# Kernel tuning notes

Hardware: AMD Instinct MI355X
Metric: run time of the kernel (lower is better)

Reference implementation:

```python
import jax, jax.numpy as jnp
import numpy as np

N = 50000      # nodes
R = 4          # relations
E = 1600000    # edges per relation
IN = 256       # in_feats
H = 256        # h_feats
C = 16         # num_classes


def setup_inputs() -> dict:
    key = jax.random.key(0)
    ks = jax.random.split(key, 8)
    X = jax.random.normal(ks[0], (N, IN), jnp.float32)
    edge_index = jax.random.randint(ks[1], (R, 2, E), 0, N, dtype=jnp.int32)
    W1 = jax.random.normal(ks[2], (R, IN, H), jnp.float32) * (1.0 / np.sqrt(IN))
    W2 = jax.random.normal(ks[3], (R, H, H), jnp.float32) * (1.0 / np.sqrt(H))
    att_q = jax.random.normal(ks[4], (H,), jnp.float32) * (1.0 / np.sqrt(H))
    tau = jnp.asarray(2.0, jnp.float32)
    W_out = jax.random.normal(ks[5], (H, C), jnp.float32) * (1.0 / np.sqrt(H))
    b_out = jnp.zeros((C,), jnp.float32)
    return {"X": X, "edge_index": edge_index, "W1": W1, "W2": W2,
            "att_q": att_q, "tau": tau, "W_out": W_out, "b_out": b_out}


def _sym_norm_spmm(edge, feat):
    """out = D^{-1/2} A D^{-1/2} @ feat for one relation, edge: [2,E]."""
    row, col = edge[0], edge[1]
    ones = jnp.ones(edge.shape[1], feat.dtype)
    deg_r = jax.ops.segment_sum(ones, row, num_segments=N)
    deg_c = jax.ops.segment_sum(ones, col, num_segments=N)
    dinv_r = jax.lax.rsqrt(jnp.maximum(deg_r, 1.0))
    dinv_c = jax.lax.rsqrt(jnp.maximum(deg_c, 1.0))
    w = dinv_r[row] * dinv_c[col]                      # [E]
    msg = w[:, None] * feat[col]                       # gather + scale
    return jax.ops.segment_sum(msg, row, num_segments=N)  # [N, F]


def _rel_layer(edge_index, feat, W):
    # vmapped over relations: ReLU(A_r feat W_r) -> [R, N, H]
    def one(edge, Wr):
        return jax.nn.relu(_sym_norm_spmm(edge, feat) @ Wr)
    return jax.vmap(one)(edge_index, W)


def reference(X, edge_index, W1, W2, att_q, tau, W_out, b_out):
    # Layer 1: mean over relations (eval mode: no dropout)
    H1 = _rel_layer(edge_index, X, W1)        # [R, N, H]
    h1 = H1.mean(axis=0)                      # [N, H]
    # Layer 2 with relation attention
    H2 = _rel_layer(edge_index, h1, W2)       # [R, N, H]
    scores = jnp.einsum('rnh,h->nr', H2, att_q)
    tau_c = jnp.clip(tau, 0.5, 5.0)
    alpha = jax.nn.softmax(scores / tau_c, axis=1)   # [N, R]
    h2_att = jnp.einsum('nr,rnh->nh', alpha, H2)
    h2 = H2.mean(axis=0) + h2_att             # residual fusion
    logits = h2 @ W_out + b_out               # [N, C]
    return logits, alpha
```

## Files before the change

### kernel.cpp

```cpp
#include <hip/hip_runtime.h>
#include <hip/hip_bf16.h>
#include <stdint.h>

#define NODES 50000
#define RELS  4
#define EDGES 1600000
#define FEAT  256
#define NCLS  16
#define MPAD  50048
#define RPS   50016
#define NCHUNK 64
#define CHUNKE 25000
#define NB     782

typedef __attribute__((ext_vector_type(8))) short short8;
typedef __attribute__((ext_vector_type(8))) unsigned short u16x8;
typedef __attribute__((ext_vector_type(4))) float f32x4;

static __device__ __forceinline__ float bf2f(unsigned short u) {
    return __uint_as_float(((unsigned int)u) << 16);
}
static __device__ __forceinline__ unsigned short f2bf(float f) {
    unsigned int x = __float_as_uint(f);
    unsigned int r = x + 0x7fffu + ((x >> 16) & 1u);
    return (unsigned short)(r >> 16);
}


__global__ __launch_bounds__(256)
void k_bhist2(const int* __restrict__ edges, unsigned* __restrict__ partR,
              unsigned* __restrict__ partC) {
    int chunk = blockIdx.x, rel = blockIdx.y, t = threadIdx.x;
    const int* rows = edges + (size_t)rel * 2 * EDGES + (size_t)chunk * CHUNKE;
    const int* cols = rows + EDGES;
    __shared__ unsigned hR[NB];
    __shared__ unsigned hC[NB];
    for (int i = t; i < NB; i += 256) { hR[i] = 0; hC[i] = 0; }
    __syncthreads();
    for (int e = t; e < CHUNKE; e += 256) {
        atomicAdd(&hR[((unsigned)rows[e]) >> 6], 1u);
        atomicAdd(&hC[((unsigned)cols[e]) >> 6], 1u);
    }
    __syncthreads();
    unsigned* pR = partR + ((size_t)rel * NCHUNK + chunk) * NB;
    unsigned* pC = partC + ((size_t)rel * NCHUNK + chunk) * NB;
    for (int i = t; i < NB; i += 256) { pR[i] = hR[i]; pC[i] = hC[i]; }
}

__global__ __launch_bounds__(256)
void k_bscan(const unsigned* __restrict__ partR, unsigned* __restrict__ offR,
             unsigned* __restrict__ bbR, const unsigned* __restrict__ partC,
             unsigned* __restrict__ offC, unsigned* __restrict__ bbC) {
    int rel = blockIdx.x & 3, t = threadIdx.x;
    const unsigned* part = (blockIdx.x < 4) ? partR : partC;
    unsigned* off   = (blockIdx.x < 4) ? offR : offC;
    unsigned* bbase = (blockIdx.x < 4) ? bbR  : bbC;
    const int BPT = 4;
    int b0 = t * BPT;
    unsigned s = 0;
#pragma unroll
    for (int j = 0; j < BPT; ++j) {
        int b = b0 + j;
        unsigned x = 0;
        if (b < NB)
            for (int c = 0; c < NCHUNK; ++c)
                x += part[((size_t)rel * NCHUNK + c) * NB + b];
        s += x;
    }
    __shared__ unsigned sh[256];
    sh[t] = s;
    __syncthreads();
    for (int o = 1; o < 256; o <<= 1) {
        unsigned u = (t >= o) ? sh[t - o] : 0;
        __syncthreads();
        sh[t] += u;
        __syncthreads();
    }
    unsigned base = sh[t] - s;
#pragma unroll
    for (int j = 0; j < BPT; ++j) {
        int b = b0 + j;
        if (b < NB) {
            bbase[rel * (NB + 1) + b] = base;
            unsigned acc = base;
            for (int c = 0; c < NCHUNK; ++c) {
                size_t o2 = ((size_t)rel * NCHUNK + c) * NB + b;
                off[o2] = acc;
                acc += part[o2];
            }
            base = acc;
        }
    }
    if (t == 255) bbase[rel * (NB + 1) + NB] = sh[255];
}

__global__ __launch_bounds__(256)
void k_scat2(const int* __restrict__ edges, const unsigned* __restrict__ offR,
             const unsigned* __restrict__ offC, unsigned* __restrict__ ebuf,
             unsigned char* __restrict__ cbuf) {
    int chunk = blockIdx.x, rel = blockIdx.y, t = threadIdx.x;
    const int* rows = edges + (size_t)rel * 2 * EDGES + (size_t)chunk * CHUNKE;
    const int* cols = rows + EDGES;
    __shared__ unsigned curR[NB];
    __shared__ unsigned curC[NB];
    const unsigned* pR = offR + ((size_t)rel * NCHUNK + chunk) * NB;
    const unsigned* pC = offC + ((size_t)rel * NCHUNK + chunk) * NB;
    for (int i = t; i < NB; i += 256) { curR[i] = pR[i]; curC[i] = pC[i]; }
    __syncthreads();
    unsigned*      eb = ebuf + (size_t)rel * EDGES;
    unsigned char* cb = cbuf + (size_t)rel * EDGES;
    for (int e = t; e < CHUNKE; e += 256) {
        int r = rows[e], c = cols[e];
        unsigned pr = atomicAdd(&curR[((unsigned)r) >> 6], 1u);
        eb[pr] = (((unsigned)(r & 63)) << 16) | (unsigned)c;
        unsigned pc = atomicAdd(&curC[((unsigned)c) >> 6], 1u);
        cb[pc] = (unsigned char)(c & 63);
    }
}

__global__ __launch_bounds__(256)
void k_finish(const unsigned* __restrict__ ebuf, const unsigned char* __restrict__ cbuf,
              const unsigned* __restrict__ bbR, const unsigned* __restrict__ bbC,
              int* __restrict__ csr_col, int* __restrict__ row_ptr,
              float* __restrict__ dinv_row, float* __restrict__ dinv_col) {
    int b = blockIdx.x, rel = blockIdx.y, t = threadIdx.x;
    unsigned sR = bbR[rel * (NB + 1) + b], eR = bbR[rel * (NB + 1) + b + 1];
    unsigned sC = bbC[rel * (NB + 1) + b], eC = bbC[rel * (NB + 1) + b + 1];
    __shared__ unsigned rcnt[64];
    __shared__ unsigned ccnt[64];
    __shared__ int cur[64];
    if (t < 64) { rcnt[t] = 0; ccnt[t] = 0; }
    __syncthreads();
    const unsigned*      eb = ebuf + (size_t)rel * EDGES;
    const unsigned char* cb = cbuf + (size_t)rel * EDGES;
    for (unsigned i = sR + t; i < eR; i += 256) atomicAdd(&rcnt[eb[i] >> 16], 1u);
    for (unsigned i = sC + t; i < eC; i += 256) atomicAdd(&ccnt[cb[i]], 1u);
    __syncthreads();
    int base = b * 64;
    if (t < 64) {
        unsigned c = rcnt[t];
        unsigned v = c;
#pragma unroll
        for (int off = 1; off < 64; off <<= 1) {
            unsigned n = __shfl_up(v, off, 64);
            if (t >= off) v += n;
        }
        unsigned excl = v - c;
        cur[t] = (int)(sR + excl);
        if (base + t < NODES) {
            row_ptr[rel * RPS + base + t] = (int)(sR + excl);
            int d = (int)c; if (d < 1) d = 1;
            dinv_row[(size_t)rel * NODES + base + t] = rsqrtf((float)d);
        }
        if (b == 0 && t == 0) row_ptr[rel * RPS + NODES] = EDGES;
    } else if (t >= 64 && t < 128) {
        int tt = t - 64;
        if (base + tt < NODES) {
            int d = (int)ccnt[tt]; if (d < 1) d = 1;
            dinv_col[(size_t)rel * NODES + base + tt] = rsqrtf((float)d);
        }
    }
    __syncthreads();
    int* cc = csr_col + (size_t)rel * EDGES;
    for (unsigned i = sR + t; i < eR; i += 256) {
        unsigned v = eb[i];
        int pos = atomicAdd(&cur[v >> 16], 1);
        cc[pos] = (int)(v & 0xFFFFu);
    }
}


#define WELEMS (2 * RELS * FEAT * FEAT)
#define XGROUPS (NODES * FEAT / 8)

__global__ __launch_bounds__(256)
void k_conv(const float* __restrict__ W1, const float* __restrict__ W2,
            unsigned short* __restrict__ W1t, unsigned short* __restrict__ W2t,
            const float* __restrict__ X, unsigned short* __restrict__ Xbf) {
    int gid = blockIdx.x * 256 + threadIdx.x;
    if (gid < WELEMS) {
        const int half = RELS * FEAT * FEAT;
        const float* W = (gid < half) ? W1 : W2;
        unsigned short* Wt = (gid < half) ? W1t : W2t;
        int id = (gid < half) ? gid : gid - half;
        int r = id >> 16;
        int rem = id & 65535;
        int n = rem >> 8;
        int k = rem & 255;
        Wt[id] = f2bf(W[(size_t)r * FEAT * FEAT + (size_t)k * FEAT + n]);
        return;
    }
    int i = gid - WELEMS;
    if (i >= XGROUPS) return;
    const float* s = X + (size_t)i * 8;
    float4 a = *(const float4*)s;
    float4 b = *(const float4*)(s + 4);
    u16x8 v;
    v[0] = f2bf(a.x); v[1] = f2bf(a.y); v[2] = f2bf(a.z); v[3] = f2bf(a.w);
    v[4] = f2bf(b.x); v[5] = f2bf(b.y); v[6] = f2bf(b.z); v[7] = f2bf(b.w);
    *(u16x8*)(Xbf + (size_t)i * 8) = v;
}


__global__ __launch_bounds__(256)
void k_spmm(const unsigned short* __restrict__ feat, const int* __restrict__ row_ptr,
            const int* __restrict__ csr_col, const float* __restrict__ dinv_row,
            const float* __restrict__ dinv_col, unsigned short* __restrict__ aggbase,
            int slice_off) {
    int rel = blockIdx.y;
    unsigned short* aggbf = aggbase + (size_t)(rel + slice_off) * (size_t)MPAD * FEAT;
    int wave = (blockIdx.x * blockDim.x + threadIdx.x) >> 6;
    int lane = threadIdx.x & 63;
    if (wave >= NODES) return;
    int row = wave;
    int half = lane >> 5;
    int l32  = lane & 31;
    int start = row_ptr[rel * RPS + row];
    int end   = row_ptr[rel * RPS + row + 1];
    const int* cols = csr_col + (size_t)rel * EDGES;
    const float* dc = dinv_col + rel * NODES;
    const unsigned short* fb = feat + l32 * 8;
    float acc[8] = {0.f, 0.f, 0.f, 0.f, 0.f, 0.f, 0.f, 0.f};
    int j = start + half;
    for (; j + 2 < end; j += 4) {
        int c0 = cols[j];
        int c1 = cols[j + 2];
        float w0 = dc[c0];
        float w1 = dc[c1];
        u16x8 u0 = *(const u16x8*)(fb + (size_t)c0 * FEAT);
        u16x8 u1 = *(const u16x8*)(fb + (size_t)c1 * FEAT);
#pragma unroll
        for (int i = 0; i < 8; ++i) acc[i] += w0 * bf2f(u0[i]);
#pragma unroll
        for (int i = 0; i < 8; ++i) acc[i] += w1 * bf2f(u1[i]);
    }
    if (j < end) {
        int c0 = cols[j];
        float w0 = dc[c0];
        u16x8 u0 = *(const u16x8*)(fb + (size_t)c0 * FEAT);
#pragma unroll
        for (int i = 0; i < 8; ++i) acc[i] += w0 * bf2f(u0[i]);
    }
#pragma unroll
    for (int i = 0; i < 8; ++i) acc[i] += __shfl_down(acc[i], 32, 64);
    if (half == 0) {
        float dr = dinv_row[rel * NODES + row];
        u16x8 o;
#pragma unroll
        for (int i = 0; i < 8; ++i) o[i] = f2bf(acc[i] * dr);
        *(u16x8*)(aggbf + (size_t)row * FEAT + l32 * 8) = o;
    }
}


__global__ __launch_bounds__(256)
void k_gemm1(const unsigned short* __restrict__ Abase, const unsigned short* __restrict__ Wt,
             unsigned short* __restrict__ h1bf) {
    __shared__ __align__(16) unsigned short As[128 * 64];
    __shared__ __align__(16) unsigned short Bs[128 * 64];
    int tid = threadIdx.x;
    int wave = tid >> 6, lane = tid & 63;
    int quad = lane >> 4, l16 = lane & 15;
    int wm = (wave & 1) * 64, wn = (wave >> 1) * 64;
    int row0 = blockIdx.x * 128, n0 = blockIdx.y * 128;

    f32x4 hacc[4][4];
#pragma unroll
    for (int mi = 0; mi < 4; ++mi)
#pragma unroll
        for (int ni = 0; ni < 4; ++ni)
            hacc[mi][ni] = (f32x4){0.f, 0.f, 0.f, 0.f};

    for (int r = 0; r < RELS; ++r) {
        const unsigned short* A  = Abase + (size_t)r * MPAD * FEAT;
        const unsigned short* Bt = Wt + (size_t)r * FEAT * FEAT;
        f32x4 acc[4][4];
#pragma unroll
        for (int mi = 0; mi < 4; ++mi)
#pragma unroll
            for (int ni = 0; ni < 4; ++ni)
                acc[mi][ni] = (f32x4){0.f, 0.f, 0.f, 0.f};

        for (int k0 = 0; k0 < FEAT; k0 += 64) {
#pragma unroll
            for (int issue = 0; issue < 4; ++issue) {
                int flat = issue * 256 + tid;
                int row = flat >> 3;
                int gr = flat & 7;
                int sg = gr ^ (row & 7);
                *(uint4*)&As[flat * 8] = *(const uint4*)(A + (size_t)(row0 + row) * FEAT + k0 + sg * 8);
                *(uint4*)&Bs[flat * 8] = *(const uint4*)(Bt + (size_t)(n0 + row) * FEAT + k0 + sg * 8);
            }
            __syncthreads();
#pragma unroll
            for (int ks = 0; ks < 2; ++ks) {
                int g = ks * 4 + quad;
                short8 af[4], bfr[4];
#pragma unroll
                for (int mi = 0; mi < 4; ++mi) {
                    int m = wm + mi * 16 + l16;
                    af[mi] = *(const short8*)&As[m * 64 + ((g ^ (m & 7)) << 3)];
                }
#pragma unroll
                for (int ni = 0; ni < 4; ++ni) {
                    int n = wn + ni * 16 + l16;
                    bfr[ni] = *(const short8*)&Bs[n * 64 + ((g ^ (n & 7)) << 3)];
                }
#pragma unroll
                for (int mi = 0; mi < 4; ++mi)
#pragma unroll
                    for (int ni = 0; ni < 4; ++ni)
                        acc[mi][ni] = __builtin_amdgcn_mfma_f32_16x16x32_bf16(af[mi], bfr[ni], acc[mi][ni], 0, 0, 0);
            }
            __syncthreads();
        }
#pragma unroll
        for (int mi = 0; mi < 4; ++mi)
#pragma unroll
            for (int ni = 0; ni < 4; ++ni)
#pragma unroll
                for (int i = 0; i < 4; ++i) {
                    float v = acc[mi][ni][i];
                    hacc[mi][ni][i] += 0.25f * (v > 0.f ? v : 0.f);
                }
    }

#pragma unroll
    for (int mi = 0; mi < 4; ++mi)
#pragma unroll
        for (int ni = 0; ni < 4; ++ni) {
            int col = n0 + wn + ni * 16 + l16;
#pragma unroll
            for (int i = 0; i < 4; ++i) {
                int row = row0 + wm + mi * 16 + quad * 4 + i;
                if (row < NODES) h1bf[(size_t)row * FEAT + col] = f2bf(hacc[mi][ni][i]);
            }
        }
}

__global__ __launch_bounds__(256)
void k_gemm2z(const unsigned short* __restrict__ aggbase, const unsigned short* __restrict__ Wtb,
              unsigned short* __restrict__ o0, unsigned short* __restrict__ o1,
              unsigned short* __restrict__ o2, unsigned short* __restrict__ o3) {
    __shared__ __align__(16) unsigned short As[128 * 64];
    __shared__ __align__(16) unsigned short Bs[128 * 64];
    int rz = blockIdx.z;
    const unsigned short* A  = aggbase + (size_t)(rz + 1) * MPAD * FEAT;
    const unsigned short* Bt = Wtb + (size_t)rz * FEAT * FEAT;
    unsigned short* H2 = (rz == 0) ? o0 : (rz == 1) ? o1 : (rz == 2) ? o2 : o3;

    int tid = threadIdx.x;
    int wave = tid >> 6, lane = tid & 63;
    int quad = lane >> 4, l16 = lane & 15;
    int wm = (wave & 1) * 64, wn = (wave >> 1) * 64;
    int row0 = blockIdx.x * 128, n0 = blockIdx.y * 128;

    f32x4 acc[4][4];
#pragma unroll
    for (int mi = 0; mi < 4; ++mi)
#pragma unroll
        for (int ni = 0; ni < 4; ++ni)
            acc[mi][ni] = (f32x4){0.f, 0.f, 0.f, 0.f};

    for (int k0 = 0; k0 < FEAT; k0 += 64) {
#pragma unroll
        for (int issue = 0; issue < 4; ++issue) {
            int flat = issue * 256 + tid;
            int row = flat >> 3;
            int gr = flat & 7;
            int sg = gr ^ (row & 7);
            *(uint4*)&As[flat * 8] = *(const uint4*)(A + (size_t)(row0 + row) * FEAT + k0 + sg * 8);
            *(uint4*)&Bs[flat * 8] = *(const uint4*)(Bt + (size_t)(n0 + row) * FEAT + k0 + sg * 8);
        }
        __syncthreads();
#pragma unroll
        for (int ks = 0; ks < 2; ++ks) {
            int g = ks * 4 + quad;
            short8 af[4], bfr[4];
#pragma unroll
            for (int mi = 0; mi < 4; ++mi) {
                int m = wm + mi * 16 + l16;
                af[mi] = *(const short8*)&As[m * 64 + ((g ^ (m & 7)) << 3)];
            }
#pragma unroll
            for (int ni = 0; ni < 4; ++ni) {
                int n = wn + ni * 16 + l16;
                bfr[ni] = *(const short8*)&Bs[n * 64 + ((g ^ (n & 7)) << 3)];
            }
#pragma unroll
            for (int mi = 0; mi < 4; ++mi)
#pragma unroll
                for (int ni = 0; ni < 4; ++ni)
                    acc[mi][ni] = __builtin_amdgcn_mfma_f32_16x16x32_bf16(af[mi], bfr[ni], acc[mi][ni], 0, 0, 0);
        }
        __syncthreads();
    }

#pragma unroll
    for (int mi = 0; mi < 4; ++mi)
#pragma unroll
        for (int ni = 0; ni < 4; ++ni) {
            int col = n0 + wn + ni * 16 + l16;
#pragma unroll
            for (int i = 0; i < 4; ++i) {
                int row = row0 + wm + mi * 16 + quad * 4 + i;
                if (row < NODES) {
                    float v = acc[mi][ni][i];
                    H2[(size_t)row * FEAT + col] = f2bf(v > 0.f ? v : 0.f);
                }
            }
        }
}


__global__ __launch_bounds__(256)
void k_attn_out(const unsigned short* __restrict__ p0, const unsigned short* __restrict__ p1,
                const unsigned short* __restrict__ p2, const unsigned short* __restrict__ p3,
                const float* __restrict__ att_q, const float* __restrict__ tau_p,
                const float* __restrict__ W_out, const float* __restrict__ b_out,
                float* __restrict__ alpha_out, float* __restrict__ logits) {
    __shared__ float red[4][64 * 17];
    int tid = threadIdx.x;
    int wid = tid >> 6;
    int lane = tid & 63;
    int gwave = blockIdx.x * 4 + wid;
    int nwaves = gridDim.x * 4;

    const unsigned short* hp[RELS] = {p0, p1, p2, p3};
    float4 q = *(const float4*)(att_q + lane * 4);
    float tau = fminf(fmaxf(tau_p[0], 0.5f), 5.0f);
    float itau = 1.0f / tau;
    f32x4 Wr[4][4];
#pragma unroll
    for (int j = 0; j < 4; ++j)
#pragma unroll
        for (int c4 = 0; c4 < 4; ++c4) {
            float4 w = *(const float4*)(W_out + (size_t)(lane * 4 + j) * NCLS + c4 * 4);
            Wr[j][c4] = (f32x4){w.x, w.y, w.z, w.w};
        }
    float bc = b_out[lane & 15];
    float* myred = &red[wid][0];
    int cls = lane & 15;
    int rb = (lane >> 4) * 16;

    int n = gwave;
    if (n >= NODES) return;
    ushort4 u[RELS];
#pragma unroll
    for (int r = 0; r < RELS; ++r)
        u[r] = *(const ushort4*)(hp[r] + (size_t)n * FEAT + lane * 4);

    while (n < NODES) {
        int nn = n + nwaves;
        int nc = (nn < NODES) ? nn : n;
        ushort4 un[RELS];
#pragma unroll
        for (int r = 0; r < RELS; ++r)
            un[r] = *(const ushort4*)(hp[r] + (size_t)nc * FEAT + lane * 4);

        float h[RELS][4];
#pragma unroll
        for (int r = 0; r < RELS; ++r) {
            h[r][0] = bf2f(u[r].x); h[r][1] = bf2f(u[r].y);
            h[r][2] = bf2f(u[r].z); h[r][3] = bf2f(u[r].w);
        }
        float s[RELS];
#pragma unroll
        for (int r = 0; r < RELS; ++r)
            s[r] = h[r][0] * q.x + h[r][1] * q.y + h[r][2] * q.z + h[r][3] * q.w;
#pragma unroll
        for (int off = 1; off < 64; off <<= 1) {
#pragma unroll
            for (int r = 0; r < RELS; ++r) s[r] += __shfl_xor(s[r], off, 64);
        }
        float m = fmaxf(fmaxf(s[0], s[1]), fmaxf(s[2], s[3]));
        float e[RELS];
        float esum = 0.f;
#pragma unroll
        for (int r = 0; r < RELS; ++r) { e[r] = expf((s[r] - m) * itau); esum += e[r]; }
        float inv = 1.0f / esum;
        float a[RELS];
#pragma unroll
        for (int r = 0; r < RELS; ++r) a[r] = e[r] * inv;
        if (lane == 0)
            *(float4*)(alpha_out + (size_t)n * 4) = make_float4(a[0], a[1], a[2], a[3]);

        float w0 = 0.25f + a[0], w1 = 0.25f + a[1], w2 = 0.25f + a[2], w3 = 0.25f + a[3];
        float h2[4];
#pragma unroll
        for (int j = 0; j < 4; ++j)
            h2[j] = w0 * h[0][j] + w1 * h[1][j] + w2 * h[2][j] + w3 * h[3][j];

        f32x4 acc[4];
#pragma unroll
        for (int c4 = 0; c4 < 4; ++c4)
            acc[c4] = h2[0] * Wr[0][c4] + h2[1] * Wr[1][c4]
                    + h2[2] * Wr[2][c4] + h2[3] * Wr[3][c4];

#pragma unroll
        for (int c4 = 0; c4 < 4; ++c4)
#pragma unroll
            for (int i = 0; i < 4; ++i)
                myred[lane * 17 + c4 * 4 + i] = acc[c4][i];
        asm volatile("s_waitcnt lgkmcnt(0)" ::: "memory");
        float t = 0.f;
#pragma unroll
        for (int k = 0; k < 16; ++k) t += myred[(rb + k) * 17 + cls];
        t += __shfl_xor(t, 16, 64);
        t += __shfl_xor(t, 32, 64);
        if (lane < 16) logits[(size_t)n * NCLS + lane] = t + bc;
        asm volatile("" ::: "memory");

#pragma unroll
        for (int r = 0; r < RELS; ++r) u[r] = un[r];
        n = nn;
    }
}


static inline int cdiv(int a, int b) { return (a + b - 1) / b; }

extern "C" void kernel_launch(void* const* d_in, const int* in_sizes, int n_in,
                              void* d_out, int out_size, void* d_ws, size_t ws_size,
                              hipStream_t stream) {
    const float* X     = (const float*)d_in[0];
    const int*   edges = (const int*)d_in[1];
    const float* W1    = (const float*)d_in[2];
    const float* W2    = (const float*)d_in[3];
    const float* att_q = (const float*)d_in[4];
    const float* tau   = (const float*)d_in[5];
    const float* W_out = (const float*)d_in[6];
    const float* b_out = (const float*)d_in[7];

    float* logits = (float*)d_out;
    float* alpha  = logits + (size_t)NODES * NCLS;

    char* p = (char*)d_ws;
    auto carve = [&](size_t bytes) -> char* {
        char* q = p;
        p += (bytes + 255) & ~(size_t)255;
        return q;
    };
    float* dinv_row = (float*)carve((size_t)RELS * NODES * 4);
    float* dinv_col = (float*)carve((size_t)RELS * NODES * 4);
    int*   row_ptr  = (int*)carve((size_t)RELS * RPS * 4 + 256);
    int*   csr_col  = (int*)carve((size_t)RELS * EDGES * 4);
    unsigned short* Xbf  = (unsigned short*)carve((size_t)NODES * FEAT * 2);
    unsigned short* h1bf = (unsigned short*)carve((size_t)NODES * FEAT * 2);
    unsigned short* W1t  = (unsigned short*)carve((size_t)RELS * FEAT * FEAT * 2);
    unsigned short* W2t  = (unsigned short*)carve((size_t)RELS * FEAT * FEAT * 2);
    const size_t AGGSE = (size_t)MPAD * FEAT;
    char* BIG = carve(5 * AGGSE * 2);
    unsigned*      ebuf = (unsigned*)BIG;
    unsigned char* cbuf = (unsigned char*)(BIG + (size_t)RELS * EDGES * 4);
    char*     q = BIG + (size_t)RELS * EDGES * 5;
    q = (char*)(((uintptr_t)q + 255) & ~(uintptr_t)255);
    unsigned* partR = (unsigned*)q;               q += (size_t)RELS * NCHUNK * NB * 4;
    unsigned* offR  = (unsigned*)q;               q += (size_t)RELS * NCHUNK * NB * 4;
    unsigned* partC = (unsigned*)q;               q += (size_t)RELS * NCHUNK * NB * 4;
    unsigned* offC  = (unsigned*)q;               q += (size_t)RELS * NCHUNK * NB * 4;
    unsigned* bbR   = (unsigned*)q;               q += (size_t)RELS * (NB + 1) * 4;
    unsigned* bbC   = (unsigned*)q;
    unsigned short* aggbf = (unsigned short*)BIG;
    unsigned short* H2_0 = aggbf;
    unsigned short* H2_1 = Xbf;
    unsigned short* H2_2 = h1bf;
    unsigned short* H2_3 = (unsigned short*)csr_col;

    {
        dim3 hg(NCHUNK, RELS);
        dim3 bg(NB, RELS);
        k_bhist2<<<hg, 256, 0, stream>>>(edges, partR, partC);
        k_bscan<<<8, 256, 0, stream>>>(partR, offR, bbR, partC, offC, bbC);
        k_scat2<<<hg, 256, 0, stream>>>(edges, offR, offC, ebuf, cbuf);
        k_finish<<<bg, 256, 0, stream>>>(ebuf, cbuf, bbR, bbC, csr_col, row_ptr,
                                         dinv_row, dinv_col);
    }

    k_conv<<<cdiv(WELEMS + XGROUPS, 256), 256, 0, stream>>>(W1, W2, W1t, W2t, X, Xbf);

    dim3 gemm_grid(MPAD / 128, FEAT / 128);
    dim3 gemm2_grid(MPAD / 128, FEAT / 128, RELS);
    dim3 spmm_grid(cdiv(NODES * 64, 256), RELS);

    k_spmm<<<spmm_grid, 256, 0, stream>>>(Xbf, row_ptr, csr_col, dinv_row, dinv_col,
                                          aggbf, 0);
    k_gemm1<<<gemm_grid, 256, 0, stream>>>(aggbf, W1t, h1bf);

    k_spmm<<<spmm_grid, 256, 0, stream>>>(h1bf, row_ptr, csr_col, dinv_row, dinv_col,
                                          aggbf, 1);
    k_gemm2z<<<gemm2_grid, 256, 0, stream>>>(aggbf, W2t, H2_0, H2_1, H2_2, H2_3);

    k_attn_out<<<1024, 256, 0, stream>>>(H2_0, H2_1, H2_2, H2_3, att_q, tau,
                                         W_out, b_out, alpha, logits);
}
```

Measured before the change: 1.379 ms.

## Fuse conversion into histogram kernel, double chunk count, use direct global-to-LDS loads

The weight/feature bf16 conversion kernel is merged into the edge histogram launch as extra blocks, removing one launch and letting conversion overlap with histogramming. The edge chunk count is doubled (half-size chunks) to raise parallelism in the histogram and scatter passes. The GEMM tile loads switch from register-staged copies to the global_load_lds builtin to cut VGPR traffic. Risks: more partial histograms for the scan to handle, and the LDS direct-load path depends on correct layout and synchronization.

```diff
diff --git a/kernel.cpp b/kernel.cpp
--- a/kernel.cpp
+++ b/kernel.cpp
@@ -9,9 +9,13 @@
 #define NCLS  16
 #define MPAD  50048
 #define RPS   50016
-#define NCHUNK 64
-#define CHUNKE 25000
+#define NCHUNK 128
+#define CHUNKE 12500
 #define NB     782
+
+#define WELEMS (2 * RELS * FEAT * FEAT)
+#define XGROUPS (NODES * FEAT / 8)
+#define CONVB  2075
 
 typedef __attribute__((ext_vector_type(8))) short short8;
 typedef __attribute__((ext_vector_type(8))) unsigned short u16x8;
@@ -26,15 +30,50 @@
     return (unsigned short)(r >> 16);
 }
 
+#define GLOAD_LDS16(gsrc, ldst)                                                          \
+    __builtin_amdgcn_global_load_lds(                                                    \
+        (const __attribute__((address_space(1))) unsigned int*)(gsrc),                   \
+        (__attribute__((address_space(3))) unsigned int*)(ldst), 16, 0, 0)
+
 
 __global__ __launch_bounds__(256)
 void k_bhist2(const int* __restrict__ edges, unsigned* __restrict__ partR,
-              unsigned* __restrict__ partC) {
-    int chunk = blockIdx.x, rel = blockIdx.y, t = threadIdx.x;
+              unsigned* __restrict__ partC,
+              const float* __restrict__ W1, const float* __restrict__ W2,
+              unsigned short* __restrict__ W1t, unsigned short* __restrict__ W2t,
+              const float* __restrict__ X, unsigned short* __restrict__ Xbf) {
+    __shared__ unsigned hR[NB];
+    __shared__ unsigned hC[NB];
+    int t = threadIdx.x;
+    if (blockIdx.x >= NCHUNK) {
+        int cid = (blockIdx.x - NCHUNK) * RELS + blockIdx.y;
+        int gid = cid * 256 + t;
+        if (gid < WELEMS) {
+            const int half = RELS * FEAT * FEAT;
+            const float* W = (gid < half) ? W1 : W2;
+            unsigned short* Wt = (gid < half) ? W1t : W2t;
+            int id = (gid < half) ? gid : gid - half;
+            int r = id >> 16;
+            int rem = id & 65535;
+            int n = rem >> 8;
+            int k = rem & 255;
+            Wt[id] = f2bf(W[(size_t)r * FEAT * FEAT + (size_t)k * FEAT + n]);
+            return;
+        }
+        int i = gid - WELEMS;
+        if (i >= XGROUPS) return;
+        const float* s = X + (size_t)i * 8;
+        float4 a = *(const float4*)s;
+        float4 b = *(const float4*)(s + 4);
+        u16x8 v;
+        v[0] = f2bf(a.x); v[1] = f2bf(a.y); v[2] = f2bf(a.z); v[3] = f2bf(a.w);
+        v[4] = f2bf(b.x); v[5] = f2bf(b.y); v[6] = f2bf(b.z); v[7] = f2bf(b.w);
+        *(u16x8*)(Xbf + (size_t)i * 8) = v;
+        return;
+    }
+    int chunk = blockIdx.x, rel = blockIdx.y;
     const int* rows = edges + (size_t)rel * 2 * EDGES + (size_t)chunk * CHUNKE;
     const int* cols = rows + EDGES;
-    __shared__ unsigned hR[NB];
-    __shared__ unsigned hC[NB];
     for (int i = t; i < NB; i += 256) { hR[i] = 0; hC[i] = 0; }
     __syncthreads();
     for (int e = t; e < CHUNKE; e += 256) {
@@ -167,38 +206,6 @@
         int pos = atomicAdd(&cur[v >> 16], 1);
         cc[pos] = (int)(v & 0xFFFFu);
     }
-}
-
-
-#define WELEMS (2 * RELS * FEAT * FEAT)
-#define XGROUPS (NODES * FEAT / 8)
-
-__global__ __launch_bounds__(256)
-void k_conv(const float* __restrict__ W1, const float* __restrict__ W2,
-            unsigned short* __restrict__ W1t, unsigned short* __restrict__ W2t,
-            const float* __restrict__ X, unsigned short* __restrict__ Xbf) {
-    int gid = blockIdx.x * 256 + threadIdx.x;
-    if (gid < WELEMS) {
-        const int half = RELS * FEAT * FEAT;
-        const float* W = (gid < half) ? W1 : W2;
-        unsigned short* Wt = (gid < half) ? W1t : W2t;
-        int id = (gid < half) ? gid : gid - half;
-        int r = id >> 16;
-        int rem = id & 65535;
-        int n = rem >> 8;
-        int k = rem & 255;
-        Wt[id] = f2bf(W[(size_t)r * FEAT * FEAT + (size_t)k * FEAT + n]);
-        return;
-    }
-    int i = gid - WELEMS;
-    if (i >= XGROUPS) return;
-    const float* s = X + (size_t)i * 8;
-    float4 a = *(const float4*)s;
-    float4 b = *(const float4*)(s + 4);
-    u16x8 v;
-    v[0] = f2bf(a.x); v[1] = f2bf(a.y); v[2] = f2bf(a.z); v[3] = f2bf(a.w);
-    v[4] = f2bf(b.x); v[5] = f2bf(b.y); v[6] = f2bf(b.z); v[7] = f2bf(b.w);
-    *(u16x8*)(Xbf + (size_t)i * 8) = v;
 }
 
 
@@ -288,8 +295,8 @@
                 int row = flat >> 3;
                 int gr = flat & 7;
                 int sg = gr ^ (row & 7);
-                *(uint4*)&As[flat * 8] = *(const uint4*)(A + (size_t)(row0 + row) * FEAT + k0 + sg * 8);
-                *(uint4*)&Bs[flat * 8] = *(const uint4*)(Bt + (size_t)(n0 + row) * FEAT + k0 + sg * 8);
+                GLOAD_LDS16(A + (size_t)(row0 + row) * FEAT + k0 + sg * 8, &As[flat * 8]);
+                GLOAD_LDS16(Bt + (size_t)(n0 + row) * FEAT + k0 + sg * 8, &Bs[flat * 8]);
             }
             __syncthreads();
 #pragma unroll
@@ -369,8 +376,8 @@
             int row = flat >> 3;
             int gr = flat & 7;
             int sg = gr ^ (row & 7);
-            *(uint4*)&As[flat * 8] = *(const uint4*)(A + (size_t)(row0 + row) * FEAT + k0 + sg * 8);
-            *(uint4*)&Bs[flat * 8] = *(const uint4*)(Bt + (size_t)(n0 + row) * FEAT + k0 + sg * 8);
+            GLOAD_LDS16(A + (size_t)(row0 + row) * FEAT + k0 + sg * 8, &As[flat * 8]);
+            GLOAD_LDS16(Bt + (size_t)(n0 + row) * FEAT + k0 + sg * 8, &Bs[flat * 8]);
         }
         __syncthreads();
 #pragma unroll
@@ -568,16 +575,15 @@
     unsigned short* H2_3 = (unsigned short*)csr_col;
 
     {
-        dim3 hg(NCHUNK, RELS);
+        dim3 hg(NCHUNK + CONVB, RELS);
+        dim3 sg(NCHUNK, RELS);
         dim3 bg(NB, RELS);
-        k_bhist2<<<hg, 256, 0, stream>>>(edges, partR, partC);
+        k_bhist2<<<hg, 256, 0, stream>>>(edges, partR, partC, W1, W2, W1t, W2t, X, Xbf);
         k_bscan<<<8, 256, 0, stream>>>(partR, offR, bbR, partC, offC, bbC);
-        k_scat2<<<hg, 256, 0, stream>>>(edges, offR, offC, ebuf, cbuf);
+        k_scat2<<<sg, 256, 0, stream>>>(edges, offR, offC, ebuf, cbuf);
         k_finish<<<bg, 256, 0, stream>>>(ebuf, cbuf, bbR, bbC, csr_col, row_ptr,
                                          dinv_row, dinv_col);
     }
-
-    k_conv<<<cdiv(WELEMS + XGROUPS, 256), 256, 0, stream>>>(W1, W2, W1t, W2t, X, Xbf);
 
     dim3 gemm_grid(MPAD / 128, FEAT / 128);
     dim3 gemm2_grid(MPAD / 128, FEAT / 128, RELS);
```

New measurement: 1.357 ms. About the same (-1.6%).
